# Kernel tuning notes

Measured on AMD Instinct MI355X. Metric: run time of the kernel, lower is better.

The kernel has to match this reference:

```python
import jax, jax.numpy as jnp
import numpy as np

IDIM = 128   # idim == odim (fc1 input dim must match shift-slice width idim_q)
HDIM = 1024
CDIM = 256
IGNORE_OUT = 10000.0


def setup_inputs() -> dict:
    key = jax.random.key(0)
    ks = jax.random.split(key, 4)
    B, T = 4, 512
    x = jax.random.normal(ks[0], (B, T, IDIM), dtype=jnp.float32)
    y = jax.random.normal(ks[1], (B, T, IDIM), dtype=jnp.float32)
    # xavier-ish init for the two linears (bias zeroed, as in initialize())
    w1 = jax.random.normal(ks[2], (HDIM, IDIM), dtype=jnp.float32) / np.sqrt(IDIM).astype(np.float32)
    b1 = jnp.zeros((HDIM,), jnp.float32)
    w2 = jax.random.normal(ks[3], (IDIM, HDIM), dtype=jnp.float32) / np.sqrt(HDIM).astype(np.float32)
    b2 = jnpts = jnp.zeros((IDIM,), jnp.float32)
    return {"x": x, "y": y, "w1": w1, "b1": b1, "w2": w2, "b2": b2}


def _shift_stack(key_seq, idim):
    """Vectorized _pad_for_shift: (B,T,idim) -> (B,T,2*idim-1,idim) shifted slices."""
    pad = idim - 1
    kp = jnp.pad(key_seq, ((0, 0), (0, 0), (pad, pad)))  # (B,T,3*idim-2)
    idx = jnp.arange(2 * idim - 1)[:, None] + jnp.arange(idim)[None, :]  # (S, idim)
    return kp[..., idx]  # (B,T,S,idim)


def _forward(x, y, w1, b1, w2, b2):
    idim = IDIM
    n_iter = HDIM // CDIM
    seq_mask = (y == IGNORE_OUT)                      # (B,T,odim)
    denom = jnp.sum(~seq_mask).astype(x.dtype)
    y_res, x_res = y, x
    losses = []
    for i in range(n_iter):
        # --- argaug (scale=False): sliding cosine cross-correlation + argmax ---
        kpt = _shift_stack(x_res, idim)               # (B,T,S,idim), S=2*idim-1
        num = jnp.einsum('btd,btsd->bts', y_res, kpt)
        den = jnp.linalg.norm(y_res, axis=-1)[..., None] * jnp.linalg.norm(kpt, axis=-1)
        sim = jnp.where(den == 0, 0.0, num / jnp.where(den == 0, 1.0, den))  # NaN(0/0) -> 0
        idx = jnp.argmax(sim, axis=-1)                # (B,T), first max like torch.max
        x_aug = jnp.take_along_axis(kpt, idx[..., None, None], axis=2)[..., 0, :]  # (B,T,idim)
        # --- attention (detached) ---
        attn = jax.lax.stop_gradient(jax.nn.softmax(x_aug * y_res, axis=-1))
        x_attn = x_aug * attn
        # --- _reverse_pad_for_shift: un-shift x_attn by 2*idim-2 - idx ---
        pad = idim - 1
        xap = jnp.pad(x_attn, ((0, 0), (0, 0), (pad, pad)))
        ridx = (2 * idim - 2 - idx)[..., None] + jnp.arange(idim)  # (B,T,idim)
        x_ele = jnp.take_along_axis(xap, ridx, axis=-1)
        # --- channel-masked two-layer MLP ---
        h = x_attn @ w1.T + b1                        # (B,T,hdim)
        m = jnp.zeros((HDIM,), x.dtype).at[i * CDIM:(i + 1) * CDIM].set(1.0)
        y_ele = (h * m) @ w2.T + b2                   # (B,T,odim)
        # --- masked MSE (sum of masked squared errors / #unmasked) ---
        sq = jnp.where(seq_mask, 0.0, (y_ele - y_res) ** 2)
        losses.append(jnp.sum(sq) / denom)
        y_res = y_res - y_ele
        x_res = x_res - x_ele
    return jnp.mean(jnp.stack(losses))


def reference(x, y, w1, b1, w2, b2):
    return _forward(x, y, w1, b1, w2, b2)
```

## Files before the change

kernel.cpp:

```cpp
#include <hip/hip_runtime.h>
#include <math.h>

#define NBLK  2048
#define NITER 4
#define IGNORE_OUT 10000.0f
#define LOG2E 1.44269504088896340736f

__device__ __forceinline__ float readlanef(float v, int lane){
  return __int_as_float(__builtin_amdgcn_readlane(__float_as_int(v), lane));
}

__device__ __forceinline__ float waveScanInc(float v){
  v += __int_as_float(__builtin_amdgcn_update_dpp(0, __float_as_int(v), 0x111, 0xF, 0xF, true));
  v += __int_as_float(__builtin_amdgcn_update_dpp(0, __float_as_int(v), 0x112, 0xF, 0xF, true));
  v += __int_as_float(__builtin_amdgcn_update_dpp(0, __float_as_int(v), 0x114, 0xF, 0xF, true));
  v += __int_as_float(__builtin_amdgcn_update_dpp(0, __float_as_int(v), 0x118, 0xF, 0xF, true));
  v += __int_as_float(__builtin_amdgcn_update_dpp(0, __float_as_int(v), 0x142, 0xA, 0xF, true));
  v += __int_as_float(__builtin_amdgcn_update_dpp(0, __float_as_int(v), 0x143, 0xC, 0xF, true));
  return v;
}
__device__ __forceinline__ float waveSum(float v){
  return readlanef(waveScanInc(v), 63);
}
__device__ __forceinline__ void waveArgmax(float &v, int &i){
#define AMSTEP(ctrl, rm) { \
    float ov = __int_as_float(__builtin_amdgcn_update_dpp(__float_as_int(v), __float_as_int(v), ctrl, rm, 0xF, false)); \
    int   oi = __builtin_amdgcn_update_dpp(i, i, ctrl, rm, 0xF, false); \
    bool take = (ov > v) || (ov == v && oi < i); \
    v = take ? ov : v; i = take ? oi : i; }
  AMSTEP(0x111, 0xF) AMSTEP(0x112, 0xF) AMSTEP(0x114, 0xF)
  AMSTEP(0x118, 0xF) AMSTEP(0x142, 0xA) AMSTEP(0x143, 0xC)
#undef AMSTEP
  v = readlanef(v, 63);
  i = __builtin_amdgcn_readlane(i, 63);
}
__device__ __forceinline__ void gatherPair(float v0, float v1, int idx, float &a, float &b){
  int c = idx & 63;
  float g0 = __shfl(v0, c, 64);
  float g1 = __shfl(v1, c, 64);
  a = ((unsigned)idx < 128u) ? ((idx & 64) ? g1 : g0) : 0.f;
  int idx2 = idx + 64;
  b = ((unsigned)idx2 < 128u) ? ((idx2 & 64) ? g1 : g0) : 0.f;
}

__global__ __launch_bounds__(512)
void prepK(const float* __restrict__ w1, const float* __restrict__ b1,
           const float* __restrict__ w2, const float* __restrict__ b2,
           float* __restrict__ M4, float* __restrict__ biasT, int* __restrict__ ticket){
  const int blk = blockIdx.x;
  const int tid = threadIdx.x;
  const int u = tid & 127, q = tid >> 7;
  __shared__ float part[512];
  if (blk < 512){
    int i = blk >> 7, o = blk & 127;
    const float* w1p = w1 + (i * 256 + q * 64) * 128 + u;
    const float* w2p = w2 + o * 1024 + i * 256 + q * 64;
    float a0 = 0.f, a1 = 0.f, a2 = 0.f, a3 = 0.f;
    #pragma unroll
    for (int c = 0; c < 64; c += 4){
      a0 = fmaf(w1p[(c + 0) * 128], w2p[c + 0], a0);
      a1 = fmaf(w1p[(c + 1) * 128], w2p[c + 1], a1);
      a2 = fmaf(w1p[(c + 2) * 128], w2p[c + 2], a2);
      a3 = fmaf(w1p[(c + 3) * 128], w2p[c + 3], a3);
    }
    part[tid] = (a0 + a1) + (a2 + a3);
    __syncthreads();
    if (q == 0)
      M4[i * 16384 + (u >> 2) * 512 + o * 4 + (u & 3)] =
          (part[u] + part[128 + u]) + (part[256 + u] + part[384 + u]);
  } else if (blk < 516){
    int i = blk - 512;
    const float* w2p = w2 + u * 1024 + i * 256 + q * 64;
    const float* b1p = b1 + i * 256 + q * 64;
    float a0 = (q == 0) ? b2[u] : 0.f, a1 = 0.f, a2 = 0.f, a3 = 0.f;
    #pragma unroll
    for (int c = 0; c < 64; c += 4){
      a0 = fmaf(b1p[c + 0], w2p[c + 0], a0);
      a1 = fmaf(b1p[c + 1], w2p[c + 1], a1);
      a2 = fmaf(b1p[c + 2], w2p[c + 2], a2);
      a3 = fmaf(b1p[c + 3], w2p[c + 3], a3);
    }
    part[tid] = (a0 + a1) + (a2 + a3);
    __syncthreads();
    if (q == 0)
      biasT[i * 128 + u] = (part[u] + part[128 + u]) + (part[256 + u] + part[384 + u]);
  } else {
    if (tid == 0) *ticket = 0;
  }
}

#define MLD(d0, d1, d2, d3, gg) \
  d0 = Mp[((gg) * 4 + 0) * 128 + u]; d1 = Mp[((gg) * 4 + 1) * 128 + u]; \
  d2 = Mp[((gg) * 4 + 2) * 128 + u]; d3 = Mp[((gg) * 4 + 3) * 128 + u];
#define MFM(m0, m1, m2, m3, src, kb) \
  a0 = fmaf((m0).x, readlanef(src, (kb) + 0), a0);  a0 = fmaf((m0).y, readlanef(src, (kb) + 1), a0); \
  a0 = fmaf((m0).z, readlanef(src, (kb) + 2), a0);  a0 = fmaf((m0).w, readlanef(src, (kb) + 3), a0); \
  a1 = fmaf((m1).x, readlanef(src, (kb) + 4), a1);  a1 = fmaf((m1).y, readlanef(src, (kb) + 5), a1); \
  a1 = fmaf((m1).z, readlanef(src, (kb) + 6), a1);  a1 = fmaf((m1).w, readlanef(src, (kb) + 7), a1); \
  a2 = fmaf((m2).x, readlanef(src, (kb) + 8), a2);  a2 = fmaf((m2).y, readlanef(src, (kb) + 9), a2); \
  a2 = fmaf((m2).z, readlanef(src, (kb) +10), a2);  a2 = fmaf((m2).w, readlanef(src, (kb) +11), a2); \
  a3 = fmaf((m3).x, readlanef(src, (kb) +12), a3);  a3 = fmaf((m3).y, readlanef(src, (kb) +13), a3); \
  a3 = fmaf((m3).z, readlanef(src, (kb) +14), a3);  a3 = fmaf((m3).w, readlanef(src, (kb) +15), a3);

__global__ __launch_bounds__(128, 4)
void mainK(const float* __restrict__ x, const float* __restrict__ y,
           const float* __restrict__ M4, const float* __restrict__ biasT,
           unsigned long long* __restrict__ partials, int* __restrict__ ticket,
           float* __restrict__ out){
  __shared__ float yd[384];
  __shared__ float sVal[2];
  __shared__ int   sIdx[2];
  __shared__ float sL[2], sC[2];
  __shared__ int   sOld;

  const int u = threadIdx.x;
  const int l = u & 63;
  const int w = u >> 6;
  const long base = (long)blockIdx.x * 128;

  float xlo = x[base + l], xhi = x[base + 64 + l];
  float ylo = y[base + l], yhi = y[base + 64 + l];
  const float yOwn0 = w ? yhi : ylo;
  const bool mOwn = (yOwn0 == IGNORE_OUT);
  float cnt = mOwn ? 0.f : 1.f;
  float lossAcc = 0.f;

  yd[128 + u] = yOwn0; yd[256 + u] = yOwn0;
  __syncthreads();

  for (int i = 0; i < NITER; ++i){
    const float4* Mp = (const float4*)(M4 + (size_t)i * 16384);

    float own2 = w ? xhi * xhi : xlo * xlo;
    float oth2 = w ? xlo * xlo : xhi * xhi;
    float v = waveScanInc(own2);
    float osum  = waveSum(oth2);
    float total = readlanef(v, 63) + osum;
    float pref_t = w ? (v + osum) : v;
    float ny2 = waveSum(ylo * ylo + yhi * yhi);

    const float* wp = yd + (255 - u);
    float s0=0.f,s1=0.f,s2=0.f,s3=0.f;
    float t0=0.f,t1=0.f,t2=0.f,t3=0.f;
    float p0=0.f,p1=0.f,p2=0.f,p3=0.f;
    if (w == 0){
      #pragma unroll
      for (int j = 0; j < 64; j += 4){
        float wv0 = wp[j], wv1 = wp[j+1], wv2 = wp[j+2], wv3 = wp[j+3];
        float x0 = readlanef(xlo, j),   x1 = readlanef(xlo, j+1);
        float x2 = readlanef(xlo, j+2), x3 = readlanef(xlo, j+3);
        s0 = fmaf(wv0, x0, s0); s1 = fmaf(wv1, x1, s1);
        s2 = fmaf(wv2, x2, s2); s3 = fmaf(wv3, x3, s3);
        p0 = fmaf((l >= j    ) ? wv0 : 0.f, x0, p0);
        p1 = fmaf((l >= j + 1) ? wv1 : 0.f, x1, p1);
        p2 = fmaf((l >= j + 2) ? wv2 : 0.f, x2, p2);
        p3 = fmaf((l >= j + 3) ? wv3 : 0.f, x3, p3);
      }
      #pragma unroll
      for (int j = 0; j < 64; j += 4){
        float wv0 = wp[64+j], wv1 = wp[64+j+1], wv2 = wp[64+j+2], wv3 = wp[64+j+3];
        t0 = fmaf(wv0, readlanef(xhi, j),   t0);
        t1 = fmaf(wv1, readlanef(xhi, j+1), t1);
        t2 = fmaf(wv2, readlanef(xhi, j+2), t2);
        t3 = fmaf(wv3, readlanef(xhi, j+3), t3);
      }
    } else {
      #pragma unroll
      for (int j = 0; j < 64; j += 4){
        float wv0 = wp[j], wv1 = wp[j+1], wv2 = wp[j+2], wv3 = wp[j+3];
        s0 = fmaf(wv0, readlanef(xlo, j),   s0);
        s1 = fmaf(wv1, readlanef(xlo, j+1), s1);
        s2 = fmaf(wv2, readlanef(xlo, j+2), s2);
        s3 = fmaf(wv3, readlanef(xlo, j+3), s3);
      }
      #pragma unroll
      for (int j = 0; j < 64; j += 4){
        float wv0 = wp[64+j], wv1 = wp[64+j+1], wv2 = wp[64+j+2], wv3 = wp[64+j+3];
        float x0 = readlanef(xhi, j),   x1 = readlanef(xhi, j+1);
        float x2 = readlanef(xhi, j+2), x3 = readlanef(xhi, j+3);
        t0 = fmaf(wv0, x0, t0); t1 = fmaf(wv1, x1, t1);
        t2 = fmaf(wv2, x2, t2); t3 = fmaf(wv3, x3, t3);
        p0 = fmaf((l >= j    ) ? wv0 : 0.f, x0, p0);
        p1 = fmaf((l >= j + 1) ? wv1 : 0.f, x1, p1);
        p2 = fmaf((l >= j + 2) ? wv2 : 0.f, x2, p2);
        p3 = fmaf((l >= j + 3) ? wv3 : 0.f, x3, p3);
      }
    }
    float Sh0 = (s0 + s1) + (s2 + s3);
    float Sh1 = (t0 + t1) + (t2 + t3);
    float P   = (p0 + p1) + (p2 + p3);
    float nt = Sh0 + Sh1;
    float n1 = w ? (Sh0 + P) : P;

    {
      bool yz = (ny2 == 0.f);
      float rNY = __builtin_amdgcn_rsqf(ny2);
      float nx2b = fmaxf(total - pref_t, 0.f);
      float s1v = (yz || pref_t == 0.f) ? 0.f : n1 * __builtin_amdgcn_rsqf(pref_t) * rNY;
      float s2v = (yz || nx2b  == 0.f) ? 0.f : (nt - n1) * __builtin_amdgcn_rsqf(nx2b) * rNY;
      if (u == 127) s2v = -INFINITY;
      float bv = s1v; int bi = u;
      if (s2v > bv){ bv = s2v; bi = u + 128; }
      waveArgmax(bv, bi);
      if (l == 0){ sVal[w] = bv; sIdx[w] = bi; }
    }
    __syncthreads();

    float4 A0, A1, A2, A3, B0, B1, B2, B3;
    MLD(A0, A1, A2, A3, 0)
    MLD(B0, B1, B2, B3, 1)
    float bias_i = biasT[i * 128 + u];

    int sstar;
    {
      float v0 = sVal[0], v1 = sVal[1];
      int   i0 = sIdx[0], i1 = sIdx[1];
      sstar = (v1 > v0 || (v1 == v0 && i1 < i0)) ? i1 : i0;
    }

    float xa, xb;
    gatherPair(xlo, xhi, sstar + l - 127, xa, xb);
    float ea = __builtin_amdgcn_exp2f(xa * ylo * LOG2E);
    float eb = __builtin_amdgcn_exp2f(xb * yhi * LOG2E);
    float rse = __builtin_amdgcn_rcpf(waveSum(ea + eb));
    float wlo = xa * (ea * rse), whi = xb * (eb * rse);

    {
      float ga, gb;
      gatherPair(wlo, whi, l + 127 - sstar, ga, gb);
      xlo -= ga; xhi -= gb;
    }

    float ye;
    {
      float a0 = 0.f, a1 = 0.f, a2 = 0.f, a3 = 0.f;
      MFM(A0, A1, A2, A3, wlo, 0)   MLD(A0, A1, A2, A3, 2)
      MFM(B0, B1, B2, B3, wlo, 16)  MLD(B0, B1, B2, B3, 3)
      MFM(A0, A1, A2, A3, wlo, 32)  MLD(A0, A1, A2, A3, 4)
      MFM(B0, B1, B2, B3, wlo, 48)  MLD(B0, B1, B2, B3, 5)
      MFM(A0, A1, A2, A3, whi, 0)   MLD(A0, A1, A2, A3, 6)
      MFM(B0, B1, B2, B3, whi, 16)  MLD(B0, B1, B2, B3, 7)
      MFM(A0, A1, A2, A3, whi, 32)
      MFM(B0, B1, B2, B3, whi, 48)
      ye = ((a0 + a1) + (a2 + a3)) + bias_i;
    }

    {
      float yOwn = w ? yhi : ylo;
      float df = ye - yOwn;
      if (!mOwn) lossAcc = fmaf(df, df, lossAcc);
      float yNew = yOwn - ye;
      yd[128 + u] = yNew; yd[256 + u] = yNew;
    }
    __syncthreads();
    ylo = yd[128 + l];
    yhi = yd[192 + l];
  }

  lossAcc = waveSum(lossAcc);
  cnt     = waveSum(cnt);
  if (l == 0){ sL[w] = lossAcc; sC[w] = cnt; }
  __syncthreads();
  if (u == 0){
    union { float2 f; unsigned long long v; } pk;
    pk.f.x = sL[0] + sL[1];
    pk.f.y = sC[0] + sC[1];
    __hip_atomic_store(&partials[blockIdx.x], pk.v, __ATOMIC_RELEASE, __HIP_MEMORY_SCOPE_AGENT);
    sOld = __hip_atomic_fetch_add(ticket, 1, __ATOMIC_ACQ_REL, __HIP_MEMORY_SCOPE_AGENT);
  }
  __syncthreads();
  if (sOld == NBLK - 1){
    float ls = 0.f, cs = 0.f;
    for (int g = u; g < NBLK; g += 128){
      union { float2 f; unsigned long long v; } pk;
      pk.v = __hip_atomic_load(&partials[g], __ATOMIC_ACQUIRE, __HIP_MEMORY_SCOPE_AGENT);
      ls += pk.f.x; cs += pk.f.y;
    }
    ls = waveSum(ls); cs = waveSum(cs);
    if (l == 0){ sL[w] = ls; sC[w] = cs; }
    __syncthreads();
    if (u == 0) out[0] = (sL[0] + sL[1]) / ((float)NITER * (sC[0] + sC[1]));
  }
}

extern "C" void kernel_launch(void* const* d_in, const int* in_sizes, int n_in,
                              void* d_out, int out_size, void* d_ws, size_t ws_size,
                              hipStream_t stream){
  const float* x  = (const float*)d_in[0];
  const float* y  = (const float*)d_in[1];
  const float* w1 = (const float*)d_in[2];
  const float* b1 = (const float*)d_in[3];
  const float* w2 = (const float*)d_in[4];
  const float* b2 = (const float*)d_in[5];
  float* out = (float*)d_out;

  int*   ticket = (int*)d_ws;
  float* M4     = (float*)((char*)d_ws + 256);
  float* biasT  = (float*)((char*)d_ws + 256 + 4 * 128 * 128 * sizeof(float));
  unsigned long long* partials =
      (unsigned long long*)((char*)d_ws + 256 + 4 * 128 * 128 * sizeof(float) + 4 * 128 * sizeof(float));

  prepK<<<517, 512, 0, stream>>>(w1, b1, w2, b2, M4, biasT, ticket);
  mainK<<<NBLK, 128, 0, stream>>>(x, y, M4, biasT, partials, ticket, out);
}
```

Before: 156.6 us.

## Replace readlane broadcasts with LDS float4 reads via skewed y copies

The sliding correlation and the MLP dot products now take x and the attention weights from per-wave LDS arrays using float4 broadcast reads, instead of hundreds of v_readlane broadcasts. The residual y is kept as four copies, each skewed by one element, so every thread's shifted window starts on a 16-byte boundary and can be read as float4. The aim is to remove the serialized scalar readlane traffic and its hazards. In exchange there are more LDS writes per y update, more LDS space per block, and more pressure on LDS bandwidth.

```diff
diff --git a/kernel.cpp b/kernel.cpp
--- a/kernel.cpp
+++ b/kernel.cpp
@@ -92,22 +92,25 @@
 #define MLD(d0, d1, d2, d3, gg) \
   d0 = Mp[((gg) * 4 + 0) * 128 + u]; d1 = Mp[((gg) * 4 + 1) * 128 + u]; \
   d2 = Mp[((gg) * 4 + 2) * 128 + u]; d3 = Mp[((gg) * 4 + 3) * 128 + u];
-#define MFM(m0, m1, m2, m3, src, kb) \
-  a0 = fmaf((m0).x, readlanef(src, (kb) + 0), a0);  a0 = fmaf((m0).y, readlanef(src, (kb) + 1), a0); \
-  a0 = fmaf((m0).z, readlanef(src, (kb) + 2), a0);  a0 = fmaf((m0).w, readlanef(src, (kb) + 3), a0); \
-  a1 = fmaf((m1).x, readlanef(src, (kb) + 4), a1);  a1 = fmaf((m1).y, readlanef(src, (kb) + 5), a1); \
-  a1 = fmaf((m1).z, readlanef(src, (kb) + 6), a1);  a1 = fmaf((m1).w, readlanef(src, (kb) + 7), a1); \
-  a2 = fmaf((m2).x, readlanef(src, (kb) + 8), a2);  a2 = fmaf((m2).y, readlanef(src, (kb) + 9), a2); \
-  a2 = fmaf((m2).z, readlanef(src, (kb) +10), a2);  a2 = fmaf((m2).w, readlanef(src, (kb) +11), a2); \
-  a3 = fmaf((m3).x, readlanef(src, (kb) +12), a3);  a3 = fmaf((m3).y, readlanef(src, (kb) +13), a3); \
-  a3 = fmaf((m3).z, readlanef(src, (kb) +14), a3);  a3 = fmaf((m3).w, readlanef(src, (kb) +15), a3);
+#define MFM(m0, m1, m2, m3, g) { \
+    float4 xA = XW[4*(g)+0], xB = XW[4*(g)+1], xC = XW[4*(g)+2], xD = XW[4*(g)+3]; \
+    a0 = fmaf((m0).x, xA.x, a0); a0 = fmaf((m0).y, xA.y, a0); \
+    a0 = fmaf((m0).z, xA.z, a0); a0 = fmaf((m0).w, xA.w, a0); \
+    a1 = fmaf((m1).x, xB.x, a1); a1 = fmaf((m1).y, xB.y, a1); \
+    a1 = fmaf((m1).z, xB.z, a1); a1 = fmaf((m1).w, xB.w, a1); \
+    a2 = fmaf((m2).x, xC.x, a2); a2 = fmaf((m2).y, xC.y, a2); \
+    a2 = fmaf((m2).z, xC.z, a2); a2 = fmaf((m2).w, xC.w, a2); \
+    a3 = fmaf((m3).x, xD.x, a3); a3 = fmaf((m3).y, xD.y, a3); \
+    a3 = fmaf((m3).z, xD.z, a3); a3 = fmaf((m3).w, xD.w, a3); }
 
 __global__ __launch_bounds__(128, 4)
 void mainK(const float* __restrict__ x, const float* __restrict__ y,
            const float* __restrict__ M4, const float* __restrict__ biasT,
            unsigned long long* __restrict__ partials, int* __restrict__ ticket,
            float* __restrict__ out){
-  __shared__ float yd[384];
+  __shared__ float ydc[4][392];
+  __shared__ float xs[2][128];
+  __shared__ float xw[2][128];
   __shared__ float sVal[2];
   __shared__ int   sIdx[2];
   __shared__ float sL[2], sC[2];
@@ -125,11 +128,19 @@
   float cnt = mOwn ? 0.f : 1.f;
   float lossAcc = 0.f;
 
-  yd[128 + u] = yOwn0; yd[256 + u] = yOwn0;
+  #pragma unroll
+  for (int r = 0; r < 4; ++r){ ydc[r][128 + u - r] = yOwn0; ydc[r][256 + u - r] = yOwn0; }
   __syncthreads();
+
+  const int A = 255 - u;
+  const float4* wrow = (const float4*)&ydc[A & 3][A & ~3];
+  const float4* XS = (const float4*)&xs[w][0];
+  const float4* XW = (const float4*)&xw[w][0];
 
   for (int i = 0; i < NITER; ++i){
     const float4* Mp = (const float4*)(M4 + (size_t)i * 16384);
+
+    xs[w][l] = xlo; xs[w][64 + l] = xhi;
 
     float own2 = w ? xhi * xhi : xlo * xlo;
     float oth2 = w ? xlo * xlo : xhi * xhi;
@@ -139,51 +150,44 @@
     float pref_t = w ? (v + osum) : v;
     float ny2 = waveSum(ylo * ylo + yhi * yhi);
 
-    const float* wp = yd + (255 - u);
     float s0=0.f,s1=0.f,s2=0.f,s3=0.f;
     float t0=0.f,t1=0.f,t2=0.f,t3=0.f;
     float p0=0.f,p1=0.f,p2=0.f,p3=0.f;
     if (w == 0){
       #pragma unroll
-      for (int j = 0; j < 64; j += 4){
-        float wv0 = wp[j], wv1 = wp[j+1], wv2 = wp[j+2], wv3 = wp[j+3];
-        float x0 = readlanef(xlo, j),   x1 = readlanef(xlo, j+1);
-        float x2 = readlanef(xlo, j+2), x3 = readlanef(xlo, j+3);
-        s0 = fmaf(wv0, x0, s0); s1 = fmaf(wv1, x1, s1);
-        s2 = fmaf(wv2, x2, s2); s3 = fmaf(wv3, x3, s3);
-        p0 = fmaf((l >= j    ) ? wv0 : 0.f, x0, p0);
-        p1 = fmaf((l >= j + 1) ? wv1 : 0.f, x1, p1);
-        p2 = fmaf((l >= j + 2) ? wv2 : 0.f, x2, p2);
-        p3 = fmaf((l >= j + 3) ? wv3 : 0.f, x3, p3);
+      for (int m = 0; m < 16; ++m){
+        float4 wv = wrow[m], xv = XS[m];
+        const int jb = 4 * m;
+        s0 = fmaf(wv.x, xv.x, s0); s1 = fmaf(wv.y, xv.y, s1);
+        s2 = fmaf(wv.z, xv.z, s2); s3 = fmaf(wv.w, xv.w, s3);
+        p0 = fmaf((l >= jb    ) ? wv.x : 0.f, xv.x, p0);
+        p1 = fmaf((l >= jb + 1) ? wv.y : 0.f, xv.y, p1);
+        p2 = fmaf((l >= jb + 2) ? wv.z : 0.f, xv.z, p2);
+        p3 = fmaf((l >= jb + 3) ? wv.w : 0.f, xv.w, p3);
       }
       #pragma unroll
-      for (int j = 0; j < 64; j += 4){
-        float wv0 = wp[64+j], wv1 = wp[64+j+1], wv2 = wp[64+j+2], wv3 = wp[64+j+3];
-        t0 = fmaf(wv0, readlanef(xhi, j),   t0);
-        t1 = fmaf(wv1, readlanef(xhi, j+1), t1);
-        t2 = fmaf(wv2, readlanef(xhi, j+2), t2);
-        t3 = fmaf(wv3, readlanef(xhi, j+3), t3);
+      for (int m = 16; m < 32; ++m){
+        float4 wv = wrow[m], xv = XS[m];
+        t0 = fmaf(wv.x, xv.x, t0); t1 = fmaf(wv.y, xv.y, t1);
+        t2 = fmaf(wv.z, xv.z, t2); t3 = fmaf(wv.w, xv.w, t3);
       }
     } else {
       #pragma unroll
-      for (int j = 0; j < 64; j += 4){
-        float wv0 = wp[j], wv1 = wp[j+1], wv2 = wp[j+2], wv3 = wp[j+3];
-        s0 = fmaf(wv0, readlanef(xlo, j),   s0);
-        s1 = fmaf(wv1, readlanef(xlo, j+1), s1);
-        s2 = fmaf(wv2, readlanef(xlo, j+2), s2);
-        s3 = fmaf(wv3, readlanef(xlo, j+3), s3);
+      for (int m = 0; m < 16; ++m){
+        float4 wv = wrow[m], xv = XS[m];
+        s0 = fmaf(wv.x, xv.x, s0); s1 = fmaf(wv.y, xv.y, s1);
+        s2 = fmaf(wv.z, xv.z, s2); s3 = fmaf(wv.w, xv.w, s3);
       }
       #pragma unroll
-      for (int j = 0; j < 64; j += 4){
-        float wv0 = wp[64+j], wv1 = wp[64+j+1], wv2 = wp[64+j+2], wv3 = wp[64+j+3];
-        float x0 = readlanef(xhi, j),   x1 = readlanef(xhi, j+1);
-        float x2 = readlanef(xhi, j+2), x3 = readlanef(xhi, j+3);
-        t0 = fmaf(wv0, x0, t0); t1 = fmaf(wv1, x1, t1);
-        t2 = fmaf(wv2, x2, t2); t3 = fmaf(wv3, x3, t3);
-        p0 = fmaf((l >= j    ) ? wv0 : 0.f, x0, p0);
-        p1 = fmaf((l >= j + 1) ? wv1 : 0.f, x1, p1);
-        p2 = fmaf((l >= j + 2) ? wv2 : 0.f, x2, p2);
-        p3 = fmaf((l >= j + 3) ? wv3 : 0.f, x3, p3);
+      for (int m = 16; m < 32; ++m){
+        float4 wv = wrow[m], xv = XS[m];
+        const int jb = 4 * m - 64;
+        t0 = fmaf(wv.x, xv.x, t0); t1 = fmaf(wv.y, xv.y, t1);
+        t2 = fmaf(wv.z, xv.z, t2); t3 = fmaf(wv.w, xv.w, t3);
+        p0 = fmaf((l >= jb    ) ? wv.x : 0.f, xv.x, p0);
+        p1 = fmaf((l >= jb + 1) ? wv.y : 0.f, xv.y, p1);
+        p2 = fmaf((l >= jb + 2) ? wv.z : 0.f, xv.z, p2);
+        p3 = fmaf((l >= jb + 3) ? wv.w : 0.f, xv.w, p3);
       }
     }
     float Sh0 = (s0 + s1) + (s2 + s3);
@@ -231,17 +235,19 @@
       xlo -= ga; xhi -= gb;
     }
 
+    xw[w][l] = wlo; xw[w][64 + l] = whi;
+
     float ye;
     {
       float a0 = 0.f, a1 = 0.f, a2 = 0.f, a3 = 0.f;
-      MFM(A0, A1, A2, A3, wlo, 0)   MLD(A0, A1, A2, A3, 2)
-      MFM(B0, B1, B2, B3, wlo, 16)  MLD(B0, B1, B2, B3, 3)
-      MFM(A0, A1, A2, A3, wlo, 32)  MLD(A0, A1, A2, A3, 4)
-      MFM(B0, B1, B2, B3, wlo, 48)  MLD(B0, B1, B2, B3, 5)
-      MFM(A0, A1, A2, A3, whi, 0)   MLD(A0, A1, A2, A3, 6)
-      MFM(B0, B1, B2, B3, whi, 16)  MLD(B0, B1, B2, B3, 7)
-      MFM(A0, A1, A2, A3, whi, 32)
-      MFM(B0, B1, B2, B3, whi, 48)
+      MFM(A0, A1, A2, A3, 0)   MLD(A0, A1, A2, A3, 2)
+      MFM(B0, B1, B2, B3, 1)   MLD(B0, B1, B2, B3, 3)
+      MFM(A0, A1, A2, A3, 2)   MLD(A0, A1, A2, A3, 4)
+      MFM(B0, B1, B2, B3, 3)   MLD(B0, B1, B2, B3, 5)
+      MFM(A0, A1, A2, A3, 4)   MLD(A0, A1, A2, A3, 6)
+      MFM(B0, B1, B2, B3, 5)   MLD(B0, B1, B2, B3, 7)
+      MFM(A0, A1, A2, A3, 6)
+      MFM(B0, B1, B2, B3, 7)
       ye = ((a0 + a1) + (a2 + a3)) + bias_i;
     }
 
@@ -250,11 +256,12 @@
       float df = ye - yOwn;
       if (!mOwn) lossAcc = fmaf(df, df, lossAcc);
       float yNew = yOwn - ye;
-      yd[128 + u] = yNew; yd[256 + u] = yNew;
-    }
-    __syncthreads();
-    ylo = yd[128 + l];
-    yhi = yd[192 + l];
+      #pragma unroll
+      for (int r = 0; r < 4; ++r){ ydc[r][128 + u - r] = yNew; ydc[r][256 + u - r] = yNew; }
+    }
+    __syncthreads();
+    ylo = ydc[0][128 + l];
+    yhi = ydc[0][192 + l];
   }
 
   lossAcc = waveSum(lossAcc);
```

Measured after the change: 176.2 us. +12.5%, slower.
